# Kernel optimization log

Measured on AMD Instinct MI355X. Metric: run time of the kernel, lower is better.

## Reference

```python
import jax, jax.numpy as jnp
import numpy as np

SCALE = 0.08838834764831845  # 1/sqrt(128)

def setup_inputs() -> dict:
    key = jax.random.key(0)
    k1, k2 = jax.random.split(key)
    x1 = jax.random.normal(k1, (16, 2048, 128), dtype=jnp.float32)
    x2 = jax.random.normal(k2, (16, 2048, 128), dtype=jnp.float32)
    return {"x1": x1, "x2": x2}

def reference(x1, x2):
    # qk = x1 @ x2^T  -> [B, Lq, Lk]
    qk = jnp.einsum('bqd,bkd->bqk', x1, x2) * SCALE
    attn = jax.nn.softmax(qk, axis=-1)
    # dropout p=0.0 -> identity
    # output = attn @ x2 (x2 doubles as values in the source module)
    out = jnp.einsum('bqk,bkd->bqd', attn, x2)
    return out
```

## Files before the change

kernel.cpp:

```cpp
#include <hip/hip_runtime.h>
#include <hip/hip_bf16.h>

typedef __attribute__((ext_vector_type(8))) short bf16x8;
typedef __attribute__((ext_vector_type(4))) float f32x4;
typedef __attribute__((ext_vector_type(4))) unsigned u32x4;
typedef __attribute__((ext_vector_type(2))) unsigned u32x2;

#define NSEQ 2048
#define DH 128
#define QBLK 128
#define KVB 64
#define QSCALE 0.12751744716167933f
#define DEFER_THR 8.0f
#define KVSTRIDE 32768

__device__ __forceinline__ unsigned cvtpk(float lo, float hi) {
  unsigned r;
  asm("v_cvt_pk_bf16_f32 %0, %1, %2" : "=v"(r) : "v"(lo), "v"(hi));
  return r;
}
__device__ __forceinline__ float fexp2(float x) { return __builtin_amdgcn_exp2f(x); }

__device__ __forceinline__ int swzT(int d) {
  return ((d & 7) ^ ((d >> 3) & 7)) << 4;
}

__global__ __launch_bounds__(256, 1) void attn_fwd(
    const float* __restrict__ x1, const float* __restrict__ x2,
    float* __restrict__ out) {
  __shared__ char lds[81920];
  char* plds = lds + 65536;

  const int tid = threadIdx.x;
  const int lane = tid & 63;
  const int wid = tid >> 6;
  const int g = lane >> 4;
  const int q15 = lane & 15;

  const int bb = blockIdx.y;
  const int qbase = blockIdx.x * QBLK + wid * 32;

  const float* x1b = x1 + (size_t)bb * NSEQ * DH;
  const float* x2b = x2 + (size_t)bb * NSEQ * DH;

  u32x4 qf[2][4];
#pragma unroll
  for (int s = 0; s < 2; ++s) {
    const float* qp = x1b + (size_t)(qbase + s * 16 + q15) * DH + g * 8;
#pragma unroll
    for (int c = 0; c < 4; ++c) {
      f32x4 v0 = *(const f32x4*)(qp + c * 32);
      f32x4 v1 = *(const f32x4*)(qp + c * 32 + 4);
      u32x4 w;
      w[0] = cvtpk(v0[0] * QSCALE, v0[1] * QSCALE);
      w[1] = cvtpk(v0[2] * QSCALE, v0[3] * QSCALE);
      w[2] = cvtpk(v1[0] * QSCALE, v1[1] * QSCALE);
      w[3] = cvtpk(v1[2] * QSCALE, v1[3] * QSCALE);
      qf[s][c] = w;
    }
  }

  const int kgrp = tid >> 4;
  const int dg = tid & 15;
  f32x4 ra[4][2];

  auto LOADRA = [&](int kv0) {
    if (kv0 < NSEQ) {
#pragma unroll
      for (int p = 0; p < 4; ++p) {
        const float* s = x2b + (size_t)(kv0 + kgrp * 4 + p) * DH + dg * 8;
        ra[p][0] = *(const f32x4*)s;
        ra[p][1] = *(const f32x4*)(s + 4);
      }
    }
  };

  auto WRITELDS = [&](int b) {
    char* kvAb = lds + b * KVSTRIDE;
    char* kvTb = kvAb + 16384;
#pragma unroll
    for (int p = 0; p < 4; ++p) {
      u32x4 w;
      w[0] = cvtpk(ra[p][0][0], ra[p][0][1]);
      w[1] = cvtpk(ra[p][0][2], ra[p][0][3]);
      w[2] = cvtpk(ra[p][1][0], ra[p][1][1]);
      w[3] = cvtpk(ra[p][1][2], ra[p][1][3]);
      const int key = kgrp * 4 + p;
      *(u32x4*)(kvAb + key * 256 + ((dg * 16) ^ ((key & 7) << 4))) = w;
    }
#pragma unroll
    for (int h = 0; h < 2; ++h)
#pragma unroll
      for (int ii = 0; ii < 4; ++ii) {
        const int d = dg * 8 + h * 4 + ii;
        u32x2 cw;
        cw[0] = cvtpk(ra[0][h][ii], ra[1][h][ii]);
        cw[1] = cvtpk(ra[2][h][ii], ra[3][h][ii]);
        *(u32x2*)(kvTb + d * 128 + ((kgrp * 8) ^ swzT(d))) = cw;
      }
  };

  float m_run[2] = {-1e30f, -1e30f};
  float l_run[2] = {0.f, 0.f};
  f32x4 o[2][8];
#pragma unroll
  for (int s = 0; s < 2; ++s)
#pragma unroll
    for (int dc = 0; dc < 8; ++dc) o[s][dc] = (f32x4){0.f, 0.f, 0.f, 0.f};

  LOADRA(0);
  WRITELDS(0);
  LOADRA(KVB);
  asm volatile("s_waitcnt lgkmcnt(0)" ::: "memory");
  __builtin_amdgcn_s_barrier();
  int cur = 0;

  for (int kv0 = 0; kv0 < NSEQ; kv0 += KVB) {
    char* kvA = lds + cur * KVSTRIDE;
    char* kvT = kvA + 16384;

    f32x4 sf[2][4];
#pragma unroll
    for (int kb = 0; kb < 4; ++kb) {
      sf[0][kb] = (f32x4){0.f, 0.f, 0.f, 0.f};
      sf[1][kb] = (f32x4){0.f, 0.f, 0.f, 0.f};
      const int key = kb * 16 + q15;
#pragma unroll
      for (int c = 0; c < 4; ++c) {
        bf16x8 a = *(const bf16x8*)(kvA + key * 256 +
                                    ((c * 64 + g * 16) ^ ((key & 7) << 4)));
        sf[0][kb] = __builtin_amdgcn_mfma_f32_16x16x32_bf16(
            a, *(const bf16x8*)&qf[0][c], sf[0][kb], 0, 0, 0);
        sf[1][kb] = __builtin_amdgcn_mfma_f32_16x16x32_bf16(
            a, *(const bf16x8*)&qf[1][c], sf[1][kb], 0, 0, 0);
      }
    }

    float mloc[2];
#pragma unroll
    for (int s = 0; s < 2; ++s) {
      float m = -1e30f;
#pragma unroll
      for (int kb = 0; kb < 4; ++kb)
#pragma unroll
        for (int r = 0; r < 4; ++r) m = fmaxf(m, sf[s][kb][r]);
      m = fmaxf(m, __shfl_xor(m, 16));
      m = fmaxf(m, __shfl_xor(m, 32));
      mloc[s] = m;
    }
    const bool ok = (mloc[0] <= m_run[0] + DEFER_THR) &&
                    (mloc[1] <= m_run[1] + DEFER_THR);
    if (!__all(ok)) {
#pragma unroll
      for (int s = 0; s < 2; ++s) {
        const float mnew = fmaxf(m_run[s], mloc[s]);
        const float corr = fexp2(m_run[s] - mnew);
#pragma unroll
        for (int dc = 0; dc < 8; ++dc) o[s][dc] *= corr;
        l_run[s] *= corr;
        m_run[s] = mnew;
      }
    }
#pragma unroll
    for (int s = 0; s < 2; ++s) {
      float tsum = 0.f;
      float pf[4][4];
#pragma unroll
      for (int kb = 0; kb < 4; ++kb)
#pragma unroll
        for (int r = 0; r < 4; ++r) {
          const float pv = fexp2(sf[s][kb][r] - m_run[s]);
          tsum += pv;
          pf[kb][r] = pv;
        }
      tsum += __shfl_xor(tsum, 16);
      tsum += __shfl_xor(tsum, 32);
      l_run[s] += tsum;
#pragma unroll
      for (int kb = 0; kb < 4; ++kb) {
        u32x2 pw;
        pw[0] = cvtpk(pf[kb][0], pf[kb][1]);
        pw[1] = cvtpk(pf[kb][2], pf[kb][3]);
        *(u32x2*)(plds + wid * 4096 + s * 2048 + q15 * 128 +
                  ((kb * 32 + g * 8) ^ ((q15 & 7) << 4))) = pw;
      }
    }

    if (kv0 + KVB < NSEQ) {
      WRITELDS(cur ^ 1);
      LOADRA(kv0 + 2 * KVB);
    }

#pragma unroll
    for (int kc = 0; kc < 2; ++kc) {
      bf16x8 pa0 = *(const bf16x8*)(plds + wid * 4096 + q15 * 128 +
                                    ((kc * 64 + g * 16) ^ ((q15 & 7) << 4)));
      bf16x8 pa1 = *(const bf16x8*)(plds + wid * 4096 + 2048 + q15 * 128 +
                                    ((kc * 64 + g * 16) ^ ((q15 & 7) << 4)));
#pragma unroll
      for (int dc = 0; dc < 8; ++dc) {
        const int d = dc * 16 + q15;
        bf16x8 vb = *(const bf16x8*)(kvT + d * 128 +
                                     ((kc * 64 + g * 16) ^ swzT(d)));
        o[0][dc] = __builtin_amdgcn_mfma_f32_16x16x32_bf16(vb, pa0, o[0][dc], 0, 0, 0);
        o[1][dc] = __builtin_amdgcn_mfma_f32_16x16x32_bf16(vb, pa1, o[1][dc], 0, 0, 0);
      }
    }

    asm volatile("s_waitcnt lgkmcnt(0)" ::: "memory");
    __builtin_amdgcn_s_barrier();
    cur ^= 1;
  }

#pragma unroll
  for (int s = 0; s < 2; ++s) {
    const float linv = 1.0f / l_run[s];
    float* op = out + (size_t)bb * NSEQ * DH + (size_t)(qbase + s * 16 + q15) * DH;
#pragma unroll
    for (int dc = 0; dc < 8; ++dc) {
      f32x4 v = o[s][dc] * linv;
      *(f32x4*)(op + dc * 16 + g * 4) = v;
    }
  }
}

extern "C" void kernel_launch(void* const* d_in, const int* in_sizes, int n_in,
                              void* d_out, int out_size, void* d_ws, size_t ws_size,
                              hipStream_t stream) {
  const float* x1 = (const float*)d_in[0];
  const float* x2 = (const float*)d_in[1];
  float* out = (float*)d_out;
  dim3 grid(NSEQ / QBLK, 16);
  attn_fwd<<<grid, dim3(256), 0, stream>>>(x1, x2, out);
}
```

Baseline: 130.7 us.

## Keep softmax probabilities in registers by permuting K rows instead of LDS round-trip

Removes the per-wave LDS staging buffer for the bf16 probability tile. Keys are written to LDS in a permuted row order so that each lane's QK^T accumulator fragments line up directly with the B-operand layout of the PV MFMA. That lets the probabilities be packed straight from registers. The change cuts LDS writes and reads plus the LDS footprint. It relies on the permutation being exactly consistent with the transposed V layout, otherwise results will be wrong.

```diff
diff --git a/kernel.cpp b/kernel.cpp
--- a/kernel.cpp
+++ b/kernel.cpp
@@ -12,7 +12,7 @@
 #define KVB 64
 #define QSCALE 0.12751744716167933f
 #define DEFER_THR 8.0f
-#define KVSTRIDE 32768
+#define KVBUF 32768
 
 __device__ __forceinline__ unsigned cvtpk(float lo, float hi) {
   unsigned r;
@@ -21,6 +21,12 @@
 }
 __device__ __forceinline__ float fexp2(float x) { return __builtin_amdgcn_exp2f(x); }
 
+__device__ __forceinline__ void wg_barrier() {
+  asm volatile("s_waitcnt lgkmcnt(0)" ::: "memory");
+  __builtin_amdgcn_s_barrier();
+  asm volatile("" ::: "memory");
+}
+
 __device__ __forceinline__ int swzT(int d) {
   return ((d & 7) ^ ((d >> 3) & 7)) << 4;
 }
@@ -28,8 +34,7 @@
 __global__ __launch_bounds__(256, 1) void attn_fwd(
     const float* __restrict__ x1, const float* __restrict__ x2,
     float* __restrict__ out) {
-  __shared__ char lds[81920];
-  char* plds = lds + 65536;
+  __shared__ char lds[65536];
 
   const int tid = threadIdx.x;
   const int lane = tid & 63;
@@ -76,7 +81,7 @@
   };
 
   auto WRITELDS = [&](int b) {
-    char* kvAb = lds + b * KVSTRIDE;
+    char* kvAb = lds + b * KVBUF;
     char* kvTb = kvAb + 16384;
 #pragma unroll
     for (int p = 0; p < 4; ++p) {
@@ -86,7 +91,8 @@
       w[2] = cvtpk(ra[p][1][0], ra[p][1][1]);
       w[3] = cvtpk(ra[p][1][2], ra[p][1][3]);
       const int key = kgrp * 4 + p;
-      *(u32x4*)(kvAb + key * 256 + ((dg * 16) ^ ((key & 7) << 4))) = w;
+      const int rho = (key & 0x23) | ((key & 4) << 2) | ((key & 0x18) >> 1);
+      *(u32x4*)(kvAb + rho * 256 + ((dg * 16) ^ ((rho & 7) << 4))) = w;
     }
 #pragma unroll
     for (int h = 0; h < 2; ++h)
@@ -111,12 +117,11 @@
   LOADRA(0);
   WRITELDS(0);
   LOADRA(KVB);
-  asm volatile("s_waitcnt lgkmcnt(0)" ::: "memory");
-  __builtin_amdgcn_s_barrier();
+  wg_barrier();
   int cur = 0;
 
   for (int kv0 = 0; kv0 < NSEQ; kv0 += KVB) {
-    char* kvA = lds + cur * KVSTRIDE;
+    char* kvA = lds + cur * KVBUF;
     char* kvT = kvA + 16384;
 
     f32x4 sf[2][4];
@@ -124,11 +129,11 @@
     for (int kb = 0; kb < 4; ++kb) {
       sf[0][kb] = (f32x4){0.f, 0.f, 0.f, 0.f};
       sf[1][kb] = (f32x4){0.f, 0.f, 0.f, 0.f};
-      const int key = kb * 16 + q15;
+      const int row = kb * 16 + q15;
 #pragma unroll
       for (int c = 0; c < 4; ++c) {
-        bf16x8 a = *(const bf16x8*)(kvA + key * 256 +
-                                    ((c * 64 + g * 16) ^ ((key & 7) << 4)));
+        bf16x8 a = *(const bf16x8*)(kvA + row * 256 +
+                                    ((c * 64 + g * 16) ^ ((row & 7) << 4)));
         sf[0][kb] = __builtin_amdgcn_mfma_f32_16x16x32_bf16(
             a, *(const bf16x8*)&qf[0][c], sf[0][kb], 0, 0, 0);
         sf[1][kb] = __builtin_amdgcn_mfma_f32_16x16x32_bf16(
@@ -136,6 +141,7 @@
       }
     }
 
+    u32x4 pa[2][2];
     float mloc[2];
 #pragma unroll
     for (int s = 0; s < 2; ++s) {
@@ -177,12 +183,13 @@
       tsum += __shfl_xor(tsum, 32);
       l_run[s] += tsum;
 #pragma unroll
-      for (int kb = 0; kb < 4; ++kb) {
-        u32x2 pw;
-        pw[0] = cvtpk(pf[kb][0], pf[kb][1]);
-        pw[1] = cvtpk(pf[kb][2], pf[kb][3]);
-        *(u32x2*)(plds + wid * 4096 + s * 2048 + q15 * 128 +
-                  ((kb * 32 + g * 8) ^ ((q15 & 7) << 4))) = pw;
+      for (int kc = 0; kc < 2; ++kc) {
+        u32x4 w;
+        w[0] = cvtpk(pf[2 * kc][0], pf[2 * kc][1]);
+        w[1] = cvtpk(pf[2 * kc][2], pf[2 * kc][3]);
+        w[2] = cvtpk(pf[2 * kc + 1][0], pf[2 * kc + 1][1]);
+        w[3] = cvtpk(pf[2 * kc + 1][2], pf[2 * kc + 1][3]);
+        pa[s][kc] = w;
       }
     }
 
@@ -193,22 +200,19 @@
 
 #pragma unroll
     for (int kc = 0; kc < 2; ++kc) {
-      bf16x8 pa0 = *(const bf16x8*)(plds + wid * 4096 + q15 * 128 +
-                                    ((kc * 64 + g * 16) ^ ((q15 & 7) << 4)));
-      bf16x8 pa1 = *(const bf16x8*)(plds + wid * 4096 + 2048 + q15 * 128 +
-                                    ((kc * 64 + g * 16) ^ ((q15 & 7) << 4)));
 #pragma unroll
       for (int dc = 0; dc < 8; ++dc) {
         const int d = dc * 16 + q15;
         bf16x8 vb = *(const bf16x8*)(kvT + d * 128 +
                                      ((kc * 64 + g * 16) ^ swzT(d)));
-        o[0][dc] = __builtin_amdgcn_mfma_f32_16x16x32_bf16(vb, pa0, o[0][dc], 0, 0, 0);
-        o[1][dc] = __builtin_amdgcn_mfma_f32_16x16x32_bf16(vb, pa1, o[1][dc], 0, 0, 0);
-      }
-    }
-
-    asm volatile("s_waitcnt lgkmcnt(0)" ::: "memory");
-    __builtin_amdgcn_s_barrier();
+        o[0][dc] = __builtin_amdgcn_mfma_f32_16x16x32_bf16(
+            vb, *(const bf16x8*)&pa[0][kc], o[0][dc], 0, 0, 0);
+        o[1][dc] = __builtin_amdgcn_mfma_f32_16x16x32_bf16(
+            vb, *(const bf16x8*)&pa[1][kc], o[1][dc], 0, 0, 0);
+      }
+    }
+
+    wg_barrier();
     cur ^= 1;
   }
 
```

After: 130.3 us. Within noise of the previous version (-0.3%).
